# Performance work log

Measured on AMD Instinct MI355X. Metric: run time of the kernel, lower is better.

The kernel has to match this reference:

```python
import jax, jax.numpy as jnp
import numpy as np

N, E, DIN, DL, DOUT, G, K = 50000, 800000, 32, 128, 10, 256, 3


def setup_inputs() -> dict:
    key = jax.random.key(0)
    ks = jax.random.split(key, 24)
    rn = lambda k, s: jax.random.normal(k, s, jnp.float32) * 0.05
    inp = {}
    inp["x"] = jax.random.normal(ks[0], (N, DIN), jnp.float32)
    inp["edge_index"] = jax.random.randint(ks[1], (2, E), 0, N, jnp.int32)
    inp["batch_ids"] = jnp.sort(jax.random.randint(ks[2], (N,), 0, G, jnp.int32))
    inp["y"] = jax.random.uniform(ks[3], (G, DOUT), dtype=jnp.float32)
    inp["eps"] = jax.random.uniform(ks[4], (K, N, DL), dtype=jnp.float32)  # torch.rand_like -> uniform
    inp["W_in"] = rn(ks[5], (DIN, DL)); inp["b_in"] = jnp.zeros((DL,), jnp.float32)
    inp["W_gcn"] = rn(ks[6], (DL, DL)); inp["b_gcn"] = jnp.zeros((DL,), jnp.float32)
    inp["W_enc"] = rn(ks[7], (5, DL, DL)); inp["b_enc"] = jnp.zeros((5, DL), jnp.float32)
    inp["W_mu"] = rn(ks[8], (DL, DL)); inp["b_mu"] = jnp.zeros((DL,), jnp.float32)
    inp["W_std"] = rn(ks[9], (DL, DL)); inp["b_std"] = jnp.zeros((DL,), jnp.float32)
    dims = [DL, 256, 128, 64, 32, 16]
    for i in range(5):
        inp[f"Wd{i}"] = rn(ks[10 + i], (dims[i], dims[i + 1]))
        inp[f"bd{i}"] = jnp.zeros((dims[i + 1],), jnp.float32)
    inp["Wo"] = rn(ks[15], (16, DOUT)); inp["bo"] = jnp.zeros((DOUT,), jnp.float32)
    inp["k"] = K
    return inp


def reference(x, edge_index, batch_ids, y, eps, W_in, b_in, W_gcn, b_gcn,
              W_enc, b_enc, W_mu, b_mu, W_std, b_std,
              Wd0, bd0, Wd1, bd1, Wd2, bd2, Wd3, bd3, Wd4, bd4, Wo, bo, k):
    n = x.shape[0]
    src, dst = edge_index[0], edge_index[1]
    # GCN symmetric normalization with self-loops (PyG gcn_norm, edge_weight=1)
    deg = jnp.zeros((n,), x.dtype).at[dst].add(1.0) + 1.0  # +1 for self-loop
    dinv = jax.lax.rsqrt(deg)
    enorm = (dinv[src] * dinv[dst])[:, None]  # [E,1]
    snorm = (dinv * dinv)[:, None]            # [N,1] self-loop norm

    h = jax.nn.sigmoid(x @ W_in + b_in)  # input layer
    mu = h; std = h
    for i in range(k):  # k hops of MPEncoder (shared weights)
        g = h @ W_gcn  # [N,DL]
        g = jax.ops.segment_sum(g[src] * enorm, dst, num_segments=n) + g * snorm + b_gcn
        for j in range(5):
            g = jax.nn.sigmoid(g @ W_enc[j] + b_enc[j])
        mu = g @ W_mu + b_mu
        std = jax.nn.softplus(g @ W_std + b_std - 5.0)
        h = mu + std * eps[i]  # reparametrization with uniform noise

    # Decoder MLP per node, sigmoid output
    d = h
    for Wd, bd in ((Wd0, bd0), (Wd1, bd1), (Wd2, bd2), (Wd3, bd3), (Wd4, bd4)):
        d = jax.nn.relu(d @ Wd + bd)
    yp = jax.nn.sigmoid(d @ Wo + bo)  # [N,DOUT]

    # global_mean_pool over graphs
    g_count = y.shape[0]
    sums = jax.ops.segment_sum(yp, batch_ids, num_segments=g_count)
    cnt = jax.ops.segment_sum(jnp.ones((n,), yp.dtype), batch_ids, num_segments=g_count)
    y_pred = sums / jnp.maximum(cnt, 1.0)[:, None]
    return (y_pred, mu, std, y)
```

## Files before the change

kernel.cpp:

```cpp
#include <hip/hip_runtime.h>
#include <math.h>

#define DIN 32
#define DL 128
#define DOUT 10

typedef _Float16 f16x8 __attribute__((ext_vector_type(8)));
typedef float f32x4 __attribute__((ext_vector_type(4)));

__device__ __forceinline__ float sigm(float x){ return 1.0f/(1.0f+expf(-x)); }
__device__ __forceinline__ float softplus_(float x){ return fmaxf(x,0.0f) + log1pf(expf(-fabsf(x))); }

__global__ void count_edges_k(const int* __restrict__ ei, int* __restrict__ cnt, int E){
    int e = blockIdx.x*256 + threadIdx.x;
    if (e < E) atomicAdd(&cnt[ei[E + e]], 1);
}

__global__ void dinv_k(const int* __restrict__ cnt, float* __restrict__ dinv, int N){
    int i = blockIdx.x*256 + threadIdx.x;
    if (i < N) dinv[i] = rsqrtf((float)cnt[i] + 1.0f);
}

__global__ void block_sum_k(const int* __restrict__ cnt, int* __restrict__ bsum, int n){
    __shared__ int ws_[4];
    int tid = threadIdx.x;
    int i = blockIdx.x*256 + tid;
    int v = (i < n) ? cnt[i] : 0;
    #pragma unroll
    for (int off = 32; off > 0; off >>= 1) v += __shfl_xor(v, off);
    if ((tid & 63) == 0) ws_[tid >> 6] = v;
    __syncthreads();
    if (tid == 0) bsum[blockIdx.x] = ws_[0] + ws_[1] + ws_[2] + ws_[3];
}

__global__ void scan_bsum_k(int* __restrict__ bsum, int nb){
    __shared__ int tmp[1024];
    int tid = threadIdx.x;
    int v = (tid < nb) ? bsum[tid] : 0;
    tmp[tid] = v; __syncthreads();
    for (int off = 1; off < 1024; off <<= 1){
        int t = (tid >= off) ? tmp[tid-off] : 0;
        __syncthreads();
        tmp[tid] += t;
        __syncthreads();
    }
    if (tid < nb) bsum[tid] = tmp[tid] - v;
}

__global__ void block_scan_k(const int* __restrict__ cnt, const int* __restrict__ bexcl,
                             int* __restrict__ cursor, int* __restrict__ rowptr, int n){
    __shared__ int tmp[256];
    int tid = threadIdx.x;
    int i = blockIdx.x*256 + tid;
    int v = (i < n) ? cnt[i] : 0;
    tmp[tid] = v; __syncthreads();
    for (int off = 1; off < 256; off <<= 1){
        int t = (tid >= off) ? tmp[tid-off] : 0;
        __syncthreads();
        tmp[tid] += t;
        __syncthreads();
    }
    int excl = bexcl[blockIdx.x] + tmp[tid] - v;
    if (i < n){ cursor[i] = excl; rowptr[i+1] = excl + v; }
    if (i == 0) rowptr[0] = 0;
}

__global__ void place_edges_k(const int* __restrict__ ei, int* __restrict__ cursor,
                              int* __restrict__ csr_src, int E){
    int e = blockIdx.x*256 + threadIdx.x;
    if (e < E){
        int s = ei[e], d = ei[E + e];
        csr_src[atomicAdd(&cursor[d], 1)] = s;
    }
}

struct WPA { const float* s; _Float16* d; int K; int C; };
struct WPA14 { WPA a[14]; };
__global__ void wprep_all_k(WPA14 args){
    WPA w = args.a[blockIdx.y];
    int idx = blockIdx.x*256 + threadIdx.x;
    if (idx < w.K*w.C){ int k = idx / w.C, c = idx % w.C; w.d[(size_t)c*w.K + k] = (_Float16)w.s[idx]; }
}

template<int K, int NC16, bool ZERO>
__device__ __forceinline__ void mfma_ldsmm(const _Float16* As, int lda,
        const _Float16* Ws, int ldw, f32x4 (&acc)[2][8], int ln, int q, int wid){
    if (ZERO){
        #pragma unroll
        for (int r = 0; r < 2; ++r)
            #pragma unroll
            for (int c = 0; c < 8; ++c) acc[r][c] = (f32x4){0.f,0.f,0.f,0.f};
    }
    #pragma unroll
    for (int kk = 0; kk < K/32; ++kk){
        int ko = kk*32 + q*8;
        f16x8 a0 = *(const f16x8*)&As[(size_t)(wid*32 + ln)*lda + ko];
        f16x8 a1 = *(const f16x8*)&As[(size_t)(wid*32 + 16 + ln)*lda + ko];
        #pragma unroll
        for (int c = 0; c < NC16; ++c){
            f16x8 b = *(const f16x8*)&Ws[(size_t)(c*16 + ln)*ldw + ko];
            acc[0][c] = __builtin_amdgcn_mfma_f32_16x16x32_f16(a0, b, acc[0][c], 0, 0, 0);
            acc[1][c] = __builtin_amdgcn_mfma_f32_16x16x32_f16(a1, b, acc[1][c], 0, 0, 0);
        }
    }
}

template<int NC16, int ACT>
__device__ __forceinline__ void act_store_lds(_Float16* D, int ldd, f32x4 (&acc)[2][8],
        const float* bias, int ln, int q, int wid){
    #pragma unroll
    for (int r = 0; r < 2; ++r){
        int rowb = wid*32 + r*16 + q*4;
        #pragma unroll
        for (int c = 0; c < NC16; ++c){
            int col = c*16 + ln;
            float bv = bias ? bias[col] : 0.0f;
            #pragma unroll
            for (int i2 = 0; i2 < 4; ++i2){
                float v = acc[r][c][i2] + bv;
                if (ACT == 1) v = sigm(v);
                else if (ACT == 2) v = fmaxf(v, 0.0f);
                D[(size_t)(rowb + i2)*ldd + col] = (_Float16)v;
            }
        }
    }
}

__device__ __forceinline__ void stage_w(const _Float16* Wg, _Float16* Wl, int ldw,
                                        int C, int K, int tid){
    int kq = K/8, tot = C*kq;
    for (int i = tid; i < tot; i += 256){
        int r = i/kq, s = i%kq;
        *(f16x8*)&Wl[(size_t)r*ldw + s*8] = *(const f16x8*)&Wg[(size_t)r*K + s*8];
    }
}

__device__ __forceinline__ void pf_load_w(const _Float16* Wg, f16x8 (&pf)[8], int tid){
    #pragma unroll
    for (int i = 0; i < 8; ++i) pf[i] = *(const f16x8*)&Wg[(size_t)(tid + i*256)*8];
}
__device__ __forceinline__ void pf_store_w(_Float16* Wl, f16x8 (&pf)[8], int tid){
    #pragma unroll
    for (int i = 0; i < 8; ++i){
        int g = tid + i*256; int r = g >> 4, s = g & 15;
        *(f16x8*)&Wl[(size_t)r*136 + s*8] = pf[i];
    }
}

__global__ __launch_bounds__(256,1) void fused_input_k(const float* __restrict__ x,
        const _Float16* __restrict__ WtIN, const float* __restrict__ b_in,
        const _Float16* __restrict__ WtGCN, _Float16* __restrict__ gOut, int nrows){
    __shared__ __align__(16) _Float16 Ax[128*40];
    __shared__ __align__(16) _Float16 Hl[128*136];
    __shared__ __align__(16) _Float16 Wi[128*40];
    __shared__ __align__(16) _Float16 Wg[128*136];
    int tid = threadIdx.x, lane = tid & 63, wid = tid >> 6;
    int ln = lane & 15, q = lane >> 4;
    int row0 = blockIdx.x * 128;
    for (int i = tid; i < 512; i += 256){
        int r = i >> 2, s = i & 3;
        f16x8 v = {};
        if (row0 + r < nrows){
            const float* xs = &x[(size_t)(row0+r)*DIN + s*8];
            float4 u0 = *(const float4*)xs, u1 = *(const float4*)(xs+4);
            v[0]=(_Float16)u0.x; v[1]=(_Float16)u0.y; v[2]=(_Float16)u0.z; v[3]=(_Float16)u0.w;
            v[4]=(_Float16)u1.x; v[5]=(_Float16)u1.y; v[6]=(_Float16)u1.z; v[7]=(_Float16)u1.w;
        }
        *(f16x8*)&Ax[r*40 + s*8] = v;
        *(f16x8*)&Wi[r*40 + s*8] = *(const f16x8*)&WtIN[(size_t)r*32 + s*8];
    }
    for (int i = tid; i < 2048; i += 256){
        int r = i >> 4, s = i & 15;
        *(f16x8*)&Wg[r*136 + s*8] = *(const f16x8*)&WtGCN[(size_t)r*128 + s*8];
    }
    __syncthreads();
    f32x4 acc[2][8];
    mfma_ldsmm<32,8,true>(Ax, 40, Wi, 40, acc, ln, q, wid);
    act_store_lds<8,1>(Hl, 136, acc, b_in, ln, q, wid);
    __syncthreads();
    mfma_ldsmm<128,8,true>(Hl, 136, Wg, 136, acc, ln, q, wid);
    #pragma unroll
    for (int r = 0; r < 2; ++r){
        int rowb = row0 + wid*32 + r*16 + q*4;
        #pragma unroll
        for (int c = 0; c < 8; ++c){
            int col = c*16 + ln;
            #pragma unroll
            for (int i2 = 0; i2 < 4; ++i2){
                int row = rowb + i2;
                if (row < nrows) gOut[(size_t)row*DL + col] = (_Float16)acc[r][c][i2];
            }
        }
    }
}

__global__ __launch_bounds__(256) void gcn_agg_h(const _Float16* __restrict__ g,
        _Float16* __restrict__ out, const int* __restrict__ rowptr,
        const int* __restrict__ csr_src, const float* __restrict__ dinv,
        const float* __restrict__ bgcn, int N){
    int t = threadIdx.x;
    int node = blockIdx.x*16 + (t >> 4);
    int f = (t & 15)*8;
    if (node >= N) return;
    float dv = dinv[node];
    float sn = dv*dv;
    f16x8 sv = *(const f16x8*)&g[(size_t)node*DL + f];
    float acc[8];
    #pragma unroll
    for (int j = 0; j < 8; ++j) acc[j] = (float)sv[j]*sn + bgcn[f+j];
    int e0 = rowptr[node], e1 = rowptr[node+1];
    for (int e = e0; e < e1; ++e){
        int s = csr_src[e];
        float w = dinv[s]*dv;
        f16x8 nv = *(const f16x8*)&g[(size_t)s*DL + f];
        #pragma unroll
        for (int j = 0; j < 8; ++j) acc[j] += (float)nv[j]*w;
    }
    f16x8 o;
    #pragma unroll
    for (int j = 0; j < 8; ++j) o[j] = (_Float16)acc[j];
    *(f16x8*)&out[(size_t)node*DL + f] = o;
}

template<int LAST>
__global__ __launch_bounds__(256,1) void fused_hop_k(const _Float16* __restrict__ g2,
        const _Float16* __restrict__ Wt8, const float* __restrict__ b_enc,
        const float* __restrict__ b_mu, const float* __restrict__ b_std,
        const float* __restrict__ eps_i, _Float16* __restrict__ gOut,
        float* __restrict__ muOut, float* __restrict__ stdOut,
        _Float16* __restrict__ hOut, int nrows){
    __shared__ __align__(16) _Float16 actA[128*136];
    __shared__ __align__(16) _Float16 actB[128*136];
    __shared__ __align__(16) _Float16 wb[2][128*136];
    int tid = threadIdx.x, lane = tid & 63, wid = tid >> 6;
    int ln = lane & 15, q = lane >> 4;
    int row0 = blockIdx.x * 128;
    for (int i = tid; i < 2048; i += 256){
        int r = i >> 4, s = i & 15;
        f16x8 v = {};
        if (row0 + r < nrows) v = *(const f16x8*)&g2[(size_t)(row0+r)*DL + s*8];
        *(f16x8*)&actA[r*136 + s*8] = v;
        *(f16x8*)&wb[0][r*136 + s*8] = *(const f16x8*)&Wt8[(size_t)1*16384 + (size_t)r*128 + s*8];
    }
    __syncthreads();
    _Float16* src = actA; _Float16* dst = actB;
    int cur = 0;
    f32x4 acc[2][8], accS[2][8];
    f16x8 pf[8];
    #pragma unroll 1
    for (int j = 0; j < 5; ++j){
        const _Float16* nxtW = Wt8 + (size_t)((j < 4) ? (2+j) : 6)*16384;
        pf_load_w(nxtW, pf, tid);
        mfma_ldsmm<128,8,true>(src, 136, wb[cur], 136, acc, ln, q, wid);
        pf_store_w(wb[cur^1], pf, tid);
        act_store_lds<8,1>(dst, 136, acc, b_enc + j*DL, ln, q, wid);
        cur ^= 1;
        { _Float16* t = src; src = dst; dst = t; }
        __syncthreads();
    }
    pf_load_w(Wt8 + (size_t)7*16384, pf, tid);
    mfma_ldsmm<128,8,true>(src, 136, wb[cur], 136, acc, ln, q, wid);
    pf_store_w(wb[cur^1], pf, tid);
    cur ^= 1;
    __syncthreads();
    if (!LAST) pf_load_w(Wt8, pf, tid);
    mfma_ldsmm<128,8,true>(src, 136, wb[cur], 136, accS, ln, q, wid);
    if (!LAST) pf_store_w(wb[cur^1], pf, tid);
    cur ^= 1;
    #pragma unroll
    for (int r = 0; r < 2; ++r){
        int rowb = wid*32 + r*16 + q*4;
        #pragma unroll
        for (int c = 0; c < 8; ++c){
            int col = c*16 + ln;
            float bm = b_mu[col], bs = b_std[col];
            #pragma unroll
            for (int i2 = 0; i2 < 4; ++i2){
                int row = rowb + i2;
                int grow = row0 + row;
                float mv = acc[r][c][i2] + bm;
                float sv = softplus_(accS[r][c][i2] + bs - 5.0f);
                float ev = (grow < nrows) ? eps_i[(size_t)grow*DL + col] : 0.0f;
                float hv = mv + sv*ev;
                if (LAST){
                    if (grow < nrows){
                        muOut[(size_t)grow*DL + col] = mv;
                        stdOut[(size_t)grow*DL + col] = sv;
                        hOut[(size_t)grow*DL + col] = (_Float16)hv;
                    }
                } else {
                    dst[(size_t)row*136 + col] = (_Float16)hv;
                }
            }
        }
    }
    if (!LAST){
        __syncthreads();
        mfma_ldsmm<128,8,true>(dst, 136, wb[cur], 136, acc, ln, q, wid);
        #pragma unroll
        for (int r = 0; r < 2; ++r){
            int rowb = row0 + wid*32 + r*16 + q*4;
            #pragma unroll
            for (int c = 0; c < 8; ++c){
                int col = c*16 + ln;
                #pragma unroll
                for (int i2 = 0; i2 < 4; ++i2){
                    int row = rowb + i2;
                    if (row < nrows) gOut[(size_t)row*DL + col] = (_Float16)acc[r][c][i2];
                }
            }
        }
    }
}

__global__ __launch_bounds__(256,1) void decoder_k(const _Float16* __restrict__ h,
        const _Float16* __restrict__ WtD0, const _Float16* __restrict__ WtD1,
        const _Float16* __restrict__ WtD2, const _Float16* __restrict__ WtD3,
        const _Float16* __restrict__ WtD4,
        const float* __restrict__ bd0, const float* __restrict__ bd1,
        const float* __restrict__ bd2, const float* __restrict__ bd3,
        const float* __restrict__ bd4, const float* __restrict__ Wo,
        const float* __restrict__ bo, const int* __restrict__ batch,
        float* __restrict__ sums, float* __restrict__ gcnt, int nrows){
    __shared__ __align__(16) _Float16 A[128*136];
    __shared__ __align__(16) _Float16 B[128*264];
    __shared__ __align__(16) _Float16 W[128*136];
    __shared__ float WoL[16*DOUT];
    __shared__ float boL[DOUT];
    int tid = threadIdx.x, lane = tid & 63, wid = tid >> 6;
    int ln = lane & 15, q = lane >> 4;
    int row0 = blockIdx.x * 128;
    for (int i = tid; i < 2048; i += 256){
        int r = i >> 4, s = i & 15;
        f16x8 v = {};
        if (row0 + r < nrows) v = *(const f16x8*)&h[(size_t)(row0+r)*DL + s*8];
        *(f16x8*)&A[r*136 + s*8] = v;
    }
    if (tid < 16*DOUT) WoL[tid] = Wo[tid];
    if (tid < DOUT) boL[tid] = bo[tid];
    f32x4 acc[2][8];
    for (int ch = 0; ch < 2; ++ch){
        stage_w(WtD0 + (size_t)ch*128*128, W, 136, 128, 128, tid);
        __syncthreads();
        mfma_ldsmm<128,8,true>(A, 136, W, 136, acc, ln, q, wid);
        act_store_lds<8,2>(B + ch*128, 264, acc, bd0 + ch*128, ln, q, wid);
        __syncthreads();
    }
    for (int kh = 0; kh < 2; ++kh){
        for (int i = tid; i < 2048; i += 256){
            int r = i >> 4, s = i & 15;
            *(f16x8*)&W[r*136 + s*8] = *(const f16x8*)&WtD1[(size_t)r*256 + kh*128 + s*8];
        }
        __syncthreads();
        if (kh == 0) mfma_ldsmm<128,8,true >(B,       264, W, 136, acc, ln, q, wid);
        else         mfma_ldsmm<128,8,false>(B + 128, 264, W, 136, acc, ln, q, wid);
        __syncthreads();
    }
    act_store_lds<8,2>(A, 136, acc, bd1, ln, q, wid);
    __syncthreads();
    stage_w(WtD2, W, 136, 64, 128, tid);
    __syncthreads();
    mfma_ldsmm<128,4,true>(A, 136, W, 136, acc, ln, q, wid);
    act_store_lds<4,2>(B, 264, acc, bd2, ln, q, wid);
    __syncthreads();
    stage_w(WtD3, W, 136, 32, 64, tid);
    __syncthreads();
    mfma_ldsmm<64,2,true>(B, 264, W, 136, acc, ln, q, wid);
    act_store_lds<2,2>(A, 136, acc, bd3, ln, q, wid);
    __syncthreads();
    stage_w(WtD4, W, 136, 16, 32, tid);
    __syncthreads();
    mfma_ldsmm<32,1,true>(A, 136, W, 136, acc, ln, q, wid);
    act_store_lds<1,2>(B, 264, acc, bd4, ln, q, wid);
    __syncthreads();
    int node = row0 + tid;
    bool valid = (tid < 128) && (node < nrows);
    float yp[DOUT];
    int b = -1;
    if (valid){
        float dd[16];
        #pragma unroll
        for (int k = 0; k < 16; ++k) dd[k] = (float)B[(size_t)tid*264 + k];
        #pragma unroll
        for (int o = 0; o < DOUT; ++o){
            float a2 = boL[o];
            #pragma unroll
            for (int k = 0; k < 16; ++k) a2 += dd[k]*WoL[k*DOUT + o];
            yp[o] = sigm(a2);
        }
        b = batch[node];
    }
    int b0 = __builtin_amdgcn_readfirstlane(b);
    unsigned long long m = __ballot(b == b0);
    if (m == ~0ull && b0 >= 0){
        #pragma unroll
        for (int o = 0; o < DOUT; ++o){
            float v = yp[o];
            for (int off = 32; off > 0; off >>= 1) v += __shfl_xor(v, off);
            if ((tid & 63) == 0) atomicAdd(&sums[b0*DOUT + o], v);
        }
        if ((tid & 63) == 0) atomicAdd(&gcnt[b0], 64.0f);
    } else if (valid){
        #pragma unroll
        for (int o = 0; o < DOUT; ++o) atomicAdd(&sums[b*DOUT + o], yp[o]);
        atomicAdd(&gcnt[b], 1.0f);
    }
}

__global__ void divide_k(float* __restrict__ out, const float* __restrict__ gcnt, int n){
    int i = blockIdx.x*256 + threadIdx.x;
    if (i < n) out[i] = out[i] / fmaxf(gcnt[i/DOUT], 1.0f);
}

__global__ void copy_k(const float* __restrict__ src, float* __restrict__ dst, int n){
    int i = blockIdx.x*256 + threadIdx.x;
    if (i < n) dst[i] = src[i];
}

extern "C" void kernel_launch(void* const* d_in, const int* in_sizes, int n_in,
                              void* d_out, int out_size, void* d_ws, size_t ws_size,
                              hipStream_t stream) {
    const float* x     = (const float*)d_in[0];
    const int*   ei    = (const int*)d_in[1];
    const int*   batch = (const int*)d_in[2];
    const float* y     = (const float*)d_in[3];
    const float* eps   = (const float*)d_in[4];
    const float* W_in  = (const float*)d_in[5];
    const float* b_in  = (const float*)d_in[6];
    const float* W_gcn = (const float*)d_in[7];
    const float* b_gcn = (const float*)d_in[8];
    const float* W_enc = (const float*)d_in[9];
    const float* b_enc = (const float*)d_in[10];
    const float* W_mu  = (const float*)d_in[11];
    const float* b_mu  = (const float*)d_in[12];
    const float* W_std = (const float*)d_in[13];
    const float* b_std = (const float*)d_in[14];
    const float* Wd0 = (const float*)d_in[15]; const float* bd0 = (const float*)d_in[16];
    const float* Wd1 = (const float*)d_in[17]; const float* bd1 = (const float*)d_in[18];
    const float* Wd2 = (const float*)d_in[19]; const float* bd2 = (const float*)d_in[20];
    const float* Wd3 = (const float*)d_in[21]; const float* bd3 = (const float*)d_in[22];
    const float* Wd4 = (const float*)d_in[23]; const float* bd4 = (const float*)d_in[24];
    const float* Wo  = (const float*)d_in[25]; const float* bo  = (const float*)d_in[26];

    const int N = in_sizes[2];
    const int E = in_sizes[1]/2;
    const int G = in_sizes[3]/DOUT;
    const int KHOP = in_sizes[4] / (N*DL);
    const size_t NN = (size_t)N*DL;

    char* p = (char*)d_ws;
    auto take = [&p](size_t bytes) -> char* {
        char* r = p; p += (bytes + 255) & ~(size_t)255; return r;
    };
    _Float16* hG  = (_Float16*)take(NN*2);
    _Float16* hG2 = (_Float16*)take(NN*2);
    _Float16* hH  = (_Float16*)take(NN*2);
    float* dinv  = (float*)take((size_t)N*4);
    float* gcnt  = (float*)take((size_t)G*4);
    int* cnt     = (int*)take((size_t)N*4);
    int* rowptr  = (int*)take((size_t)(N+1)*4);
    int* cursor  = (int*)take((size_t)N*4);
    int* csr_src = (int*)take((size_t)E*4);
    int* bsum    = (int*)take(1024*4);
    _Float16* Wt8  = (_Float16*)take((size_t)8*DL*DL*2);
    _Float16* WtIN = (_Float16*)take((size_t)DL*DIN*2);
    _Float16* WtD0 = (_Float16*)take((size_t)256*128*2);
    _Float16* WtD1 = (_Float16*)take((size_t)128*256*2);
    _Float16* WtD2 = (_Float16*)take((size_t)64*128*2);
    _Float16* WtD3 = (_Float16*)take((size_t)32*64*2);
    _Float16* WtD4 = (_Float16*)take((size_t)16*32*2);

    float* out_ypred = (float*)d_out;
    float* out_mu    = out_ypred + (size_t)G*DOUT;
    float* out_std   = out_mu + NN;
    float* out_y     = out_std + NN;

    hipMemsetAsync(cnt, 0, sizeof(int)*N, stream);
    hipMemsetAsync(out_ypred, 0, sizeof(float)*G*DOUT, stream);
    hipMemsetAsync(gcnt, 0, sizeof(float)*G, stream);

    int gE = (E + 255)/256, gN = (N + 255)/256;
    int nb = gN;

    count_edges_k<<<gE, 256, 0, stream>>>(ei, cnt, E);
    dinv_k<<<gN, 256, 0, stream>>>(cnt, dinv, N);
    block_sum_k<<<nb, 256, 0, stream>>>(cnt, bsum, N);
    scan_bsum_k<<<1, 1024, 0, stream>>>(bsum, nb);
    block_scan_k<<<nb, 256, 0, stream>>>(cnt, bsum, cursor, rowptr, N);
    place_edges_k<<<gE, 256, 0, stream>>>(ei, cursor, csr_src, E);

    WPA14 wa;
    wa.a[0]  = { W_in,  WtIN, DIN, DL };
    wa.a[1]  = { W_gcn, Wt8,  DL, DL };
    for (int j = 0; j < 5; ++j) wa.a[2+j] = { W_enc + (size_t)j*DL*DL, Wt8 + (size_t)(1+j)*DL*DL, DL, DL };
    wa.a[7]  = { W_mu,  Wt8 + (size_t)6*DL*DL, DL, DL };
    wa.a[8]  = { W_std, Wt8 + (size_t)7*DL*DL, DL, DL };
    wa.a[9]  = { Wd0, WtD0, 128, 256 };
    wa.a[10] = { Wd1, WtD1, 256, 128 };
    wa.a[11] = { Wd2, WtD2, 128, 64 };
    wa.a[12] = { Wd3, WtD3, 64, 32 };
    wa.a[13] = { Wd4, WtD4, 32, 16 };
    wprep_all_k<<<dim3(128, 14), 256, 0, stream>>>(wa);

    int ntile = (N + 127)/128;
    fused_input_k<<<ntile, 256, 0, stream>>>(x, WtIN, b_in, Wt8, hG, N);

    for (int i = 0; i < KHOP; ++i){
        gcn_agg_h<<<(N+15)/16, 256, 0, stream>>>(hG, hG2, rowptr, csr_src, dinv, b_gcn, N);
        const float* eps_i = eps + (size_t)i*NN;
        if (i == KHOP-1)
            fused_hop_k<1><<<ntile, 256, 0, stream>>>(hG2, Wt8, b_enc, b_mu, b_std, eps_i,
                                                      nullptr, out_mu, out_std, hH, N);
        else
            fused_hop_k<0><<<ntile, 256, 0, stream>>>(hG2, Wt8, b_enc, b_mu, b_std, eps_i,
                                                      hG, nullptr, nullptr, nullptr, N);
    }

    decoder_k<<<ntile, 256, 0, stream>>>(hH, WtD0, WtD1, WtD2, WtD3, WtD4,
                                         bd0, bd1, bd2, bd3, bd4, Wo, bo,
                                         batch, out_ypred, gcnt, N);
    divide_k<<<(G*DOUT+255)/256, 256, 0, stream>>>(out_ypred, gcnt, G*DOUT);
    copy_k<<<(G*DOUT+255)/256, 256, 0, stream>>>(y, out_y, G*DOUT);
}
```

Baseline: 969.8 us.

## Shrink hop kernel LDS to two buffers for 2 blocks/CU; unroll GCN gather

The per-hop MLP kernel drops its ping-pong activation buffers and double-buffered weight prefetch. It now keeps one activation tile and one weight tile in LDS (about 70KB instead of about 140KB), so two blocks can be resident per CU under launch_bounds(256,2). Mu and std are computed in sequence, with std*eps held in registers as fp16, and each matmul is fenced by synchronous weight staging. The GCN aggregation loop is unrolled by four so more neighbor gathers are in flight. The cost is losing the weight-load/MFMA overlap inside a block, adding barriers, and slightly lower precision for std*eps.

```diff
diff --git a/kernel.cpp b/kernel.cpp
--- a/kernel.cpp
+++ b/kernel.cpp
@@ -132,18 +132,6 @@
     for (int i = tid; i < tot; i += 256){
         int r = i/kq, s = i%kq;
         *(f16x8*)&Wl[(size_t)r*ldw + s*8] = *(const f16x8*)&Wg[(size_t)r*K + s*8];
-    }
-}
-
-__device__ __forceinline__ void pf_load_w(const _Float16* Wg, f16x8 (&pf)[8], int tid){
-    #pragma unroll
-    for (int i = 0; i < 8; ++i) pf[i] = *(const f16x8*)&Wg[(size_t)(tid + i*256)*8];
-}
-__device__ __forceinline__ void pf_store_w(_Float16* Wl, f16x8 (&pf)[8], int tid){
-    #pragma unroll
-    for (int i = 0; i < 8; ++i){
-        int g = tid + i*256; int r = g >> 4, s = g & 15;
-        *(f16x8*)&Wl[(size_t)r*136 + s*8] = pf[i];
     }
 }
 
@@ -208,8 +196,19 @@
     float acc[8];
     #pragma unroll
     for (int j = 0; j < 8; ++j) acc[j] = (float)sv[j]*sn + bgcn[f+j];
-    int e0 = rowptr[node], e1 = rowptr[node+1];
-    for (int e = e0; e < e1; ++e){
+    int e = rowptr[node], e1 = rowptr[node+1];
+    for (; e + 4 <= e1; e += 4){
+        int s0 = csr_src[e], s1 = csr_src[e+1], s2 = csr_src[e+2], s3 = csr_src[e+3];
+        float w0 = dinv[s0]*dv, w1 = dinv[s1]*dv, w2 = dinv[s2]*dv, w3 = dinv[s3]*dv;
+        f16x8 n0 = *(const f16x8*)&g[(size_t)s0*DL + f];
+        f16x8 n1 = *(const f16x8*)&g[(size_t)s1*DL + f];
+        f16x8 n2 = *(const f16x8*)&g[(size_t)s2*DL + f];
+        f16x8 n3 = *(const f16x8*)&g[(size_t)s3*DL + f];
+        #pragma unroll
+        for (int j = 0; j < 8; ++j)
+            acc[j] += (float)n0[j]*w0 + (float)n1[j]*w1 + (float)n2[j]*w2 + (float)n3[j]*w3;
+    }
+    for (; e < e1; ++e){
         int s = csr_src[e];
         float w = dinv[s]*dv;
         f16x8 nv = *(const f16x8*)&g[(size_t)s*DL + f];
@@ -223,15 +222,14 @@
 }
 
 template<int LAST>
-__global__ __launch_bounds__(256,1) void fused_hop_k(const _Float16* __restrict__ g2,
+__global__ __launch_bounds__(256,2) void hop2_k(const _Float16* __restrict__ g2,
         const _Float16* __restrict__ Wt8, const float* __restrict__ b_enc,
         const float* __restrict__ b_mu, const float* __restrict__ b_std,
         const float* __restrict__ eps_i, _Float16* __restrict__ gOut,
         float* __restrict__ muOut, float* __restrict__ stdOut,
         _Float16* __restrict__ hOut, int nrows){
-    __shared__ __align__(16) _Float16 actA[128*136];
-    __shared__ __align__(16) _Float16 actB[128*136];
-    __shared__ __align__(16) _Float16 wb[2][128*136];
+    __shared__ __align__(16) _Float16 Act[128*136];
+    __shared__ __align__(16) _Float16 Wb[128*136];
     int tid = threadIdx.x, lane = tid & 63, wid = tid >> 6;
     int ln = lane & 15, q = lane >> 4;
     int row0 = blockIdx.x * 128;
@@ -239,64 +237,67 @@
         int r = i >> 4, s = i & 15;
         f16x8 v = {};
         if (row0 + r < nrows) v = *(const f16x8*)&g2[(size_t)(row0+r)*DL + s*8];
-        *(f16x8*)&actA[r*136 + s*8] = v;
-        *(f16x8*)&wb[0][r*136 + s*8] = *(const f16x8*)&Wt8[(size_t)1*16384 + (size_t)r*128 + s*8];
-    }
-    __syncthreads();
-    _Float16* src = actA; _Float16* dst = actB;
-    int cur = 0;
-    f32x4 acc[2][8], accS[2][8];
-    f16x8 pf[8];
+        *(f16x8*)&Act[r*136 + s*8] = v;
+    }
+    f32x4 acc[2][8];
+    auto stageW = [&](int m){
+        __syncthreads();
+        stage_w(Wt8 + (size_t)m*16384, Wb, 136, 128, 128, tid);
+        __syncthreads();
+    };
     #pragma unroll 1
     for (int j = 0; j < 5; ++j){
-        const _Float16* nxtW = Wt8 + (size_t)((j < 4) ? (2+j) : 6)*16384;
-        pf_load_w(nxtW, pf, tid);
-        mfma_ldsmm<128,8,true>(src, 136, wb[cur], 136, acc, ln, q, wid);
-        pf_store_w(wb[cur^1], pf, tid);
-        act_store_lds<8,1>(dst, 136, acc, b_enc + j*DL, ln, q, wid);
-        cur ^= 1;
-        { _Float16* t = src; src = dst; dst = t; }
-        __syncthreads();
-    }
-    pf_load_w(Wt8 + (size_t)7*16384, pf, tid);
-    mfma_ldsmm<128,8,true>(src, 136, wb[cur], 136, acc, ln, q, wid);
-    pf_store_w(wb[cur^1], pf, tid);
-    cur ^= 1;
-    __syncthreads();
-    if (!LAST) pf_load_w(Wt8, pf, tid);
-    mfma_ldsmm<128,8,true>(src, 136, wb[cur], 136, accS, ln, q, wid);
-    if (!LAST) pf_store_w(wb[cur^1], pf, tid);
-    cur ^= 1;
+        stageW(1+j);
+        mfma_ldsmm<128,8,true>(Act, 136, Wb, 136, acc, ln, q, wid);
+        act_store_lds<8,1>(Act, 136, acc, b_enc + j*DL, ln, q, wid);
+    }
+    stageW(7);
+    mfma_ldsmm<128,8,true>(Act, 136, Wb, 136, acc, ln, q, wid);
+    f16x8 se[2][4];
     #pragma unroll
     for (int r = 0; r < 2; ++r){
-        int rowb = wid*32 + r*16 + q*4;
+        int rowb = row0 + wid*32 + r*16 + q*4;
         #pragma unroll
         for (int c = 0; c < 8; ++c){
             int col = c*16 + ln;
-            float bm = b_mu[col], bs = b_std[col];
+            float bs = b_std[col];
             #pragma unroll
             for (int i2 = 0; i2 < 4; ++i2){
-                int row = rowb + i2;
-                int grow = row0 + row;
+                int grow = rowb + i2;
+                float s = softplus_(acc[r][c][i2] + bs - 5.0f);
+                float ev = (grow < nrows) ? eps_i[(size_t)grow*DL + col] : 0.0f;
+                int fi = c*4 + i2;
+                se[r][fi>>3][fi&7] = (_Float16)(s*ev);
+                if (LAST && grow < nrows) stdOut[(size_t)grow*DL + col] = s;
+            }
+        }
+    }
+    stageW(6);
+    mfma_ldsmm<128,8,true>(Act, 136, Wb, 136, acc, ln, q, wid);
+    #pragma unroll
+    for (int r = 0; r < 2; ++r){
+        int rowl = wid*32 + r*16 + q*4;
+        #pragma unroll
+        for (int c = 0; c < 8; ++c){
+            int col = c*16 + ln;
+            float bm = b_mu[col];
+            #pragma unroll
+            for (int i2 = 0; i2 < 4; ++i2){
+                int grow = row0 + rowl + i2;
                 float mv = acc[r][c][i2] + bm;
-                float sv = softplus_(accS[r][c][i2] + bs - 5.0f);
-                float ev = (grow < nrows) ? eps_i[(size_t)grow*DL + col] : 0.0f;
-                float hv = mv + sv*ev;
-                if (LAST){
-                    if (grow < nrows){
-                        muOut[(size_t)grow*DL + col] = mv;
-                        stdOut[(size_t)grow*DL + col] = sv;
-                        hOut[(size_t)grow*DL + col] = (_Float16)hv;
-                    }
-                } else {
-                    dst[(size_t)row*136 + col] = (_Float16)hv;
+                int fi = c*4 + i2;
+                float hv = mv + (float)se[r][fi>>3][fi&7];
+                Act[(size_t)(rowl + i2)*136 + col] = (_Float16)hv;
+                if (LAST && grow < nrows){
+                    muOut[(size_t)grow*DL + col] = mv;
+                    hOut[(size_t)grow*DL + col] = (_Float16)hv;
                 }
             }
         }
     }
     if (!LAST){
-        __syncthreads();
-        mfma_ldsmm<128,8,true>(dst, 136, wb[cur], 136, acc, ln, q, wid);
+        stageW(0);
+        mfma_ldsmm<128,8,true>(Act, 136, Wb, 136, acc, ln, q, wid);
         #pragma unroll
         for (int r = 0; r < 2; ++r){
             int rowb = row0 + wid*32 + r*16 + q*4;
@@ -305,8 +306,8 @@
                 int col = c*16 + ln;
                 #pragma unroll
                 for (int i2 = 0; i2 < 4; ++i2){
-                    int row = rowb + i2;
-                    if (row < nrows) gOut[(size_t)row*DL + col] = (_Float16)acc[r][c][i2];
+                    int grow = rowb + i2;
+                    if (grow < nrows) gOut[(size_t)grow*DL + col] = (_Float16)acc[r][c][i2];
                 }
             }
         }
@@ -509,11 +510,11 @@
         gcn_agg_h<<<(N+15)/16, 256, 0, stream>>>(hG, hG2, rowptr, csr_src, dinv, b_gcn, N);
         const float* eps_i = eps + (size_t)i*NN;
         if (i == KHOP-1)
-            fused_hop_k<1><<<ntile, 256, 0, stream>>>(hG2, Wt8, b_enc, b_mu, b_std, eps_i,
-                                                      nullptr, out_mu, out_std, hH, N);
+            hop2_k<1><<<ntile, 256, 0, stream>>>(hG2, Wt8, b_enc, b_mu, b_std, eps_i,
+                                                 nullptr, out_mu, out_std, hH, N);
         else
-            fused_hop_k<0><<<ntile, 256, 0, stream>>>(hG2, Wt8, b_enc, b_mu, b_std, eps_i,
-                                                      hG, nullptr, nullptr, nullptr, N);
+            hop2_k<0><<<ntile, 256, 0, stream>>>(hG2, Wt8, b_enc, b_mu, b_std, eps_i,
+                                                 hG, nullptr, nullptr, nullptr, N);
     }
 
     decoder_k<<<ntile, 256, 0, stream>>>(hH, WtD0, WtD1, WtD2, WtD3, WtD4,
```

Result: faster. 793.5 us (-18.2%).
